# Optimization experiments

Measured on AMD Instinct MI355X. Metric: run time of the kernel, lower is better.

Reference implementation:

```python
import jax, jax.numpy as jnp
import numpy as np

N = 100_000
E = 1_000_000
D = 64
NORM_FACTOR = 100.0
LN_EPS = 1e-5


def setup_inputs() -> dict:
    key = jax.random.key(0)
    ks = jax.random.split(key, 8)
    h = jax.random.normal(ks[0], (N, D), dtype=jnp.float32)
    distances = jax.random.uniform(ks[1], (E, 1), dtype=jnp.float32)
    edges = jax.random.randint(ks[2], (2, E), 0, N, dtype=jnp.int64)
    node_mask = jnp.ones((N, 1), dtype=jnp.float32)
    edge_mask = jnp.ones((E, 1), dtype=jnp.float32)
    s = 1.0 / np.sqrt(D)
    W_lin = jax.random.normal(ks[3], (D, D), dtype=jnp.float32) * s
    b_lin = jnp.zeros((D,), dtype=jnp.float32)
    att_W1 = jax.random.normal(ks[4], (D, 2 * D + 1), dtype=jnp.float32) * (1.0 / np.sqrt(2 * D + 1))
    att_b1 = jnp.zeros((D,), dtype=jnp.float32)
    att_W2 = jax.random.normal(ks[5], (1, D), dtype=jnp.float32) * s
    att_b2 = jnp.zeros((1,), dtype=jnp.float32)
    ln_g = jnp.ones((D,), dtype=jnp.float32)
    ln_b = jnp.zeros((D,), dtype=jnp.float32)
    return {"h": h, "distances": distances, "edges": edges, "node_mask": node_mask,
            "edge_mask": edge_mask, "W_lin": W_lin, "b_lin": b_lin,
            "att_W1": att_W1, "att_b1": att_b1, "att_W2": att_W2, "att_b2": att_b2,
            "ln_g": ln_g, "ln_b": ln_b}


def reference(h, distances, edges, node_mask, edge_mask, W_lin, b_lin,
              att_W1, att_b1, att_W2, att_b2, ln_g, ln_b):
    # Linear projection: [N, D]
    x = h @ W_lin.T + b_lin
    row, col = edges[0], edges[1]
    x_row = x[row]          # [E, D]
    x_col = x[col]          # [E, D]
    # DenseAtt: MLP(concat(x_row, x_col, dist)) -> sigmoid -> * edge_mask
    cat = jnp.concatenate([x_row, x_col, distances], axis=1)  # [E, 2D+1]
    hdn = jax.nn.silu(cat @ att_W1.T + att_b1)                # [E, D]
    att = jax.nn.sigmoid(hdn @ att_W2.T + att_b2) * edge_mask # [E, 1]
    # Attention-weighted scatter-sum aggregation into row segments
    agg = x_col * att
    out = jax.ops.segment_sum(agg, row, num_segments=x.shape[0]) / NORM_FACTOR
    out = out + x           # residual
    # LayerNorm + activation
    mu = jnp.mean(out, axis=-1, keepdims=True)
    var = jnp.mean(jnp.square(out - mu), axis=-1, keepdims=True)
    y = (out - mu) * jax.lax.rsqrt(var + LN_EPS) * ln_g + ln_b
    return jax.nn.silu(y)
```

## Files before the change

### kernel.cpp

```cpp
#include <hip/hip_runtime.h>
#include <hip/hip_bf16.h>

#define N_NODES 100000
#define N_EDGES 1000000
#define DIM 64
#define NORM_INV 0.01f
#define LN_EPS 1e-5f
#define N_TILES 6250
#define PROJ_BLOCKS 1563
#define N_BUCKETS 782
#define HISTB 489
#define L2E 1.4426950408889634f
#define LN2 0.6931471805599453f

typedef __attribute__((ext_vector_type(8))) short short8;
typedef __attribute__((ext_vector_type(4))) float f32x4;

__device__ __forceinline__ unsigned short f2bf(float f) {
    union { float f; unsigned u; } x; x.f = f;
    unsigned r = x.u + 0x7FFFu + ((x.u >> 16) & 1u);
    return (unsigned short)(r >> 16);
}
__device__ __forceinline__ float bf2f(unsigned short s) {
    union { unsigned u; float f; } x; x.u = ((unsigned)s) << 16; return x.f;
}

__global__ __launch_bounds__(256) void prep_frags(
    const float* __restrict__ W, const float* __restrict__ att_W1,
    const float* __restrict__ att_b1, const float* __restrict__ att_W2,
    short8* __restrict__ whi, short8* __restrict__ wlo,
    short8* __restrict__ wa, short8* __restrict__ wb,
    float4* __restrict__ tab) {
    const int l = threadIdx.x & 63;
    const int nt = threadIdx.x >> 6;
    const int c = l & 15, q = l >> 4;
    const int n = nt * 16 + c;
#pragma unroll
    for (int ks = 0; ks < 2; ++ks) {
        const int k0 = ks * 32 + q * 8;
        short8 hi8, lo8, a8, b8;
#pragma unroll
        for (int jj = 0; jj < 8; ++jj) {
            float w = W[n * 64 + k0 + jj];
            unsigned short hh = f2bf(w);
            hi8[jj] = (short)hh;
            lo8[jj] = (short)f2bf(w - bf2f(hh));
            a8[jj] = (short)f2bf(att_W1[n * 129 + k0 + jj]);
            b8[jj] = (short)f2bf(att_W1[n * 129 + 64 + k0 + jj]);
        }
        const int idx = (nt * 2 + ks) * 64 + l;
        whi[idx] = hi8; wlo[idx] = lo8; wa[idx] = a8; wb[idx] = b8;
    }
    if (threadIdx.x < 64) {
        const int f = threadIdx.x;
        tab[f] = make_float4(att_W2[f] * LN2, att_W1[f * 129 + 128] * L2E,
                             att_b1[f] * L2E, 0.f);
    }
}

__global__ __launch_bounds__(256) void proj_hist(
    const float* __restrict__ h, const float* __restrict__ bl,
    const short8* __restrict__ whi, const short8* __restrict__ wlo,
    const short8* __restrict__ wa, const short8* __restrict__ wb,
    const int* __restrict__ edges, int* __restrict__ bucketCnt,
    unsigned short* __restrict__ xv, unsigned short* __restrict__ u_bf) {
    if (blockIdx.x >= PROJ_BLOCKS) {
        __shared__ int lh[N_BUCKETS];
        const int tid = threadIdx.x;
        for (int i = tid; i < N_BUCKETS; i += 256) lh[i] = 0;
        __syncthreads();
        const int e0 = (blockIdx.x - PROJ_BLOCKS) * 2048;
#pragma unroll
        for (int i = 0; i < 8; ++i) {
            const int e = e0 + tid * 8 + i;
            if (e < N_EDGES) atomicAdd(&lh[edges[e] >> 7], 1);
        }
        __syncthreads();
        for (int b = tid; b < N_BUCKETS; b += 256)
            if (lh[b]) atomicAdd(&bucketCnt[b], lh[b]);
        return;
    }
    __shared__ __align__(16) unsigned short lds[4][16 * 72];
    const int lane = threadIdx.x & 63;
    const int wv = threadIdx.x >> 6;
    const int c = lane & 15, q = lane >> 4;
    const int tile = blockIdx.x * 4 + wv;
    if (tile >= N_TILES) return;
    const int n0 = tile * 16;

    short8 Whi[4][2], Wlo[4][2], Wa[4][2], Wb[4][2];
    float bias[4];
#pragma unroll
    for (int nt = 0; nt < 4; ++nt) {
        bias[nt] = bl[nt * 16 + c];
#pragma unroll
        for (int ks = 0; ks < 2; ++ks) {
            const int idx = (nt * 2 + ks) * 64 + lane;
            Whi[nt][ks] = whi[idx]; Wlo[nt][ks] = wlo[idx];
            Wa[nt][ks] = wa[idx];   Wb[nt][ks] = wb[idx];
        }
    }

    short8 Ahi[2], Alo[2];
#pragma unroll
    for (int ks = 0; ks < 2; ++ks) {
        const float* hp = h + (size_t)(n0 + c) * 64 + ks * 32 + q * 8;
        f32x4 p0 = *(const f32x4*)hp;
        f32x4 p1 = *(const f32x4*)(hp + 4);
        short8 hi8, lo8;
#pragma unroll
        for (int jj = 0; jj < 4; ++jj) {
            unsigned short hh = f2bf(p0[jj]);
            hi8[jj] = (short)hh; lo8[jj] = (short)f2bf(p0[jj] - bf2f(hh));
            unsigned short h2 = f2bf(p1[jj]);
            hi8[4 + jj] = (short)h2; lo8[4 + jj] = (short)f2bf(p1[jj] - bf2f(h2));
        }
        Ahi[ks] = hi8; Alo[ks] = lo8;
    }

    f32x4 xacc[4] = {{0,0,0,0},{0,0,0,0},{0,0,0,0},{0,0,0,0}};
#pragma unroll
    for (int ks = 0; ks < 2; ++ks)
#pragma unroll
        for (int nt = 0; nt < 4; ++nt) {
            xacc[nt] = __builtin_amdgcn_mfma_f32_16x16x32_bf16(Ahi[ks], Whi[nt][ks], xacc[nt], 0, 0, 0);
            xacc[nt] = __builtin_amdgcn_mfma_f32_16x16x32_bf16(Ahi[ks], Wlo[nt][ks], xacc[nt], 0, 0, 0);
            xacc[nt] = __builtin_amdgcn_mfma_f32_16x16x32_bf16(Alo[ks], Whi[nt][ks], xacc[nt], 0, 0, 0);
        }

    unsigned short* lw = lds[wv];
#pragma unroll
    for (int r = 0; r < 4; ++r) {
        const int node = n0 + q * 4 + r;
        unsigned short xb[4];
#pragma unroll
        for (int nt = 0; nt < 4; ++nt) {
            unsigned short v16 = f2bf(xacc[nt][r] + bias[nt]);
            xb[nt] = v16;
            lw[(q * 4 + r) * 72 + nt * 16 + c] = v16;
        }
        uint2 pk;
        pk.x = (unsigned)xb[0] | ((unsigned)xb[1] << 16);
        pk.y = (unsigned)xb[2] | ((unsigned)xb[3] << 16);
        *(uint2*)(xv + (size_t)node * 128 + c * 8) = pk;
    }

    short8 Ax[2];
#pragma unroll
    for (int ks = 0; ks < 2; ++ks)
        Ax[ks] = *(const short8*)&lw[c * 72 + ks * 32 + q * 8];

    f32x4 uacc[4] = {{0,0,0,0},{0,0,0,0},{0,0,0,0},{0,0,0,0}};
    f32x4 vacc[4] = {{0,0,0,0},{0,0,0,0},{0,0,0,0},{0,0,0,0}};
#pragma unroll
    for (int ks = 0; ks < 2; ++ks)
#pragma unroll
        for (int nt = 0; nt < 4; ++nt) {
            uacc[nt] = __builtin_amdgcn_mfma_f32_16x16x32_bf16(Ax[ks], Wa[nt][ks], uacc[nt], 0, 0, 0);
            vacc[nt] = __builtin_amdgcn_mfma_f32_16x16x32_bf16(Ax[ks], Wb[nt][ks], vacc[nt], 0, 0, 0);
        }
#pragma unroll
    for (int r = 0; r < 4; ++r) {
        const int node = n0 + q * 4 + r;
        uint2 pu;
        pu.x = (unsigned)f2bf(uacc[0][r] * L2E) | ((unsigned)f2bf(uacc[1][r] * L2E) << 16);
        pu.y = (unsigned)f2bf(uacc[2][r] * L2E) | ((unsigned)f2bf(uacc[3][r] * L2E) << 16);
        *(uint2*)(u_bf + (size_t)node * 64 + c * 4) = pu;
        uint2 pk;
        pk.x = (unsigned)f2bf(vacc[0][r] * L2E) | ((unsigned)f2bf(vacc[1][r] * L2E) << 16);
        pk.y = (unsigned)f2bf(vacc[2][r] * L2E) | ((unsigned)f2bf(vacc[3][r] * L2E) << 16);
        *(uint2*)(xv + (size_t)node * 128 + c * 8 + 4) = pk;
    }
}

__global__ __launch_bounds__(1024) void scanA(
    const int* __restrict__ bucketCnt, int* __restrict__ baseA,
    int* __restrict__ cursA) {
    __shared__ int wsum[16];
    const int t = threadIdx.x, lane = t & 63, w = t >> 6;
    const int v = (t < N_BUCKETS) ? bucketCnt[t] : 0;
    int sc = v;
#pragma unroll
    for (int off = 1; off < 64; off <<= 1) {
        int u = __shfl_up(sc, off);
        if (lane >= off) sc += u;
    }
    if (lane == 63) wsum[w] = sc;
    __syncthreads();
    if (w == 0) {
        int x = (lane < 16) ? wsum[lane] : 0;
#pragma unroll
        for (int off = 1; off < 16; off <<= 1) {
            int u = __shfl_up(x, off);
            if (lane >= off) x += u;
        }
        if (lane < 16) wsum[lane] = x;
    }
    __syncthreads();
    const int excl = sc - v + ((w > 0) ? wsum[w - 1] : 0);
    if (t < N_BUCKETS) { baseA[t] = excl; cursA[t] = excl; }
    if (t == N_BUCKETS - 1) baseA[N_BUCKETS] = excl + v;
}

__global__ __launch_bounds__(256) void scatterA(
    const int* __restrict__ edges, const float* __restrict__ dist,
    const float* __restrict__ emask, int* __restrict__ cursA,
    uint2* __restrict__ srec, unsigned char* __restrict__ lrowS) {
    __shared__ int lh[N_BUCKETS];
    __shared__ int lb[N_BUCKETS];
    const int tid = threadIdx.x;
    for (int i = tid; i < N_BUCKETS; i += 256) lh[i] = 0;
    __syncthreads();

    const int e0 = blockIdx.x * 2048 + tid * 8;
    int row[8], col[8];
    unsigned de[8];
#pragma unroll
    for (int i = 0; i < 8; ++i) {
        const int e = e0 + i;
        if (e < N_EDGES) {
            row[i] = edges[e];
            col[i] = edges[N_EDGES + e];
            de[i] = (unsigned)f2bf(dist[e]) | ((unsigned)f2bf(emask[e] * NORM_INV) << 16);
            atomicAdd(&lh[row[i] >> 7], 1);
        } else {
            row[i] = -1;
        }
    }
    __syncthreads();
    for (int b = tid; b < N_BUCKETS; b += 256) {
        const int c = lh[b];
        lb[b] = c ? atomicAdd(&cursA[b], c) : 0;
    }
    __syncthreads();
    for (int i = tid; i < N_BUCKETS; i += 256) lh[i] = 0;
    __syncthreads();
#pragma unroll
    for (int i = 0; i < 8; ++i) {
        if (row[i] >= 0) {
            const int bk = row[i] >> 7;
            const int rk = atomicAdd(&lh[bk], 1);
            const int pos = lb[bk] + rk;
            uint2 rc; rc.x = (unsigned)col[i]; rc.y = de[i];
            srec[pos] = rc;
            lrowS[pos] = (unsigned char)(row[i] & 127);
        }
    }
}

__global__ __launch_bounds__(256) void bucketB1(
    const int* __restrict__ baseA, const unsigned char* __restrict__ lrowS,
    int* __restrict__ pbt) {
    __shared__ int hist[128];
    __shared__ int tt[4];
    const int tid = threadIdx.x;
    const int b = blockIdx.x;
    if (tid < 128) hist[tid] = 0;
    __syncthreads();
    const int s0 = baseA[b], s1 = baseA[b + 1];
    for (int e = s0 + tid; e < s1; e += 256) atomicAdd(&hist[lrowS[e]], 1);
    __syncthreads();
    int p = (tid < 128) ? ((hist[tid] + 3) & ~3) : 0;
#pragma unroll
    for (int off = 1; off < 64; off <<= 1) p += __shfl_xor(p, off);
    if ((tid & 63) == 0) tt[tid >> 6] = p;
    __syncthreads();
    if (tid == 0) pbt[b] = tt[0] + tt[1];
}

__global__ __launch_bounds__(1024) void scanB(
    const int* __restrict__ pbt, int* __restrict__ baseB,
    int* __restrict__ start, uint2* __restrict__ recs) {
    __shared__ int wsum[16];
    const int t = threadIdx.x, lane = t & 63, w = t >> 6;
    const int v = (t < N_BUCKETS) ? pbt[t] : 0;
    int sc = v;
#pragma unroll
    for (int off = 1; off < 64; off <<= 1) {
        int u = __shfl_up(sc, off);
        if (lane >= off) sc += u;
    }
    if (lane == 63) wsum[w] = sc;
    __syncthreads();
    if (w == 0) {
        int x = (lane < 16) ? wsum[lane] : 0;
#pragma unroll
        for (int off = 1; off < 16; off <<= 1) {
            int u = __shfl_up(x, off);
            if (lane >= off) x += u;
        }
        if (lane < 16) wsum[lane] = x;
    }
    __syncthreads();
    const int excl = sc - v + ((w > 0) ? wsum[w - 1] : 0);
    if (t < N_BUCKETS) baseB[t] = excl;
    if (t == N_BUCKETS - 1) {
        const int tot = excl + v;
        baseB[N_BUCKETS] = tot;
        start[N_NODES] = tot;
        uint2 z; z.x = 0; z.y = 0;
        for (int i = 0; i < 16; ++i) recs[tot + i] = z;
    }
}

__global__ __launch_bounds__(256) void bucketB2(
    const int* __restrict__ baseA, const int* __restrict__ baseB,
    const unsigned char* __restrict__ lrowS, const uint2* __restrict__ srec,
    uint2* __restrict__ recs, int* __restrict__ start) {
    __shared__ int hist[128];
    __shared__ int cur[128];
    __shared__ int wtot;
    const int tid = threadIdx.x, lane = tid & 63;
    const int b = blockIdx.x;
    if (tid < 128) hist[tid] = 0;
    __syncthreads();
    const int s0 = baseA[b], s1 = baseA[b + 1];
    for (int e = s0 + tid; e < s1; e += 256) atomicAdd(&hist[lrowS[e]], 1);
    __syncthreads();
    int c = 0, p = 0, sc = 0;
    if (tid < 128) {
        c = hist[tid];
        p = (c + 3) & ~3;
        sc = p;
#pragma unroll
        for (int off = 1; off < 64; off <<= 1) {
            int u = __shfl_up(sc, off);
            if (lane >= off) sc += u;
        }
        if (tid == 63) wtot = sc;
    }
    __syncthreads();
    if (tid < 128) {
        if (tid >= 64) sc += wtot;
        const int excl = baseB[b] + sc - p;
        cur[tid] = excl;
        const int grow = b * 128 + tid;
        if (grow < N_NODES) start[grow] = excl;
        uint2 z; z.x = 0; z.y = 0;
        for (int i = c; i < p; ++i) recs[excl + i] = z;
    }
    __syncthreads();
    for (int e = s0 + tid; e < s1; e += 256) {
        const int lr = lrowS[e];
        const uint2 rc = srec[e];
        const int pos = atomicAdd(&cur[lr], 1);
        recs[pos] = rc;
    }
}

__global__ __launch_bounds__(256, 8) void agg_ln_kernel(
    const int* __restrict__ start, const uint2* __restrict__ recs,
    const unsigned short* __restrict__ xv, const unsigned short* __restrict__ u_bf,
    const float4* __restrict__ tab, const float* __restrict__ att_b2,
    const float* __restrict__ ln_g, const float* __restrict__ ln_b,
    float* __restrict__ out) {
    const int lane = threadIdx.x & 63;
    const int wv = threadIdx.x >> 6;
    const int j = lane & 15;
    const int s = lane >> 4;
    const int r = blockIdx.x * 4 + wv;

    const float4 t0 = tab[j], t1 = tab[j + 16], t2 = tab[j + 32], t3 = tab[j + 48];
    const uint2 uu = *(const uint2*)(u_bf + (size_t)r * 64 + j * 4);
    const float base0 = __uint_as_float(uu.x << 16) + t0.z;
    const float base1 = __uint_as_float(uu.x & 0xffff0000u) + t1.z;
    const float base2 = __uint_as_float(uu.y << 16) + t2.z;
    const float base3 = __uint_as_float(uu.y & 0xffff0000u) + t3.z;
    const float b2L = att_b2[0] * L2E;

    const int s0 = start[r];
    const int e1 = start[r + 1];
    const unsigned* xvu = (const unsigned*)xv;

    float a0 = 0.f, a1 = 0.f, a2 = 0.f, a3 = 0.f;
    if (e1 > s0) {
        uint2 recA = recs[s0 + s];
        uint4 xvA = *(const uint4*)(xvu + (size_t)recA.x * 64 + j * 4);
        uint2 recB = recs[s0 + 4 + s];
        for (int e = s0; e < e1; e += 4) {
            const uint2 recC = recs[e + 8 + s];
            const uint4 xvB = *(const uint4*)(xvu + (size_t)recB.x * 64 + j * 4);

            const float dist = __uint_as_float(recA.y << 16);
            const float emN = __uint_as_float(recA.y & 0xffff0000u);
            const float x0 = __uint_as_float(xvA.x << 16);
            const float x1 = __uint_as_float(xvA.x & 0xffff0000u);
            const float x2 = __uint_as_float(xvA.y << 16);
            const float x3 = __uint_as_float(xvA.y & 0xffff0000u);
            const float v0 = __uint_as_float(xvA.z << 16);
            const float v1 = __uint_as_float(xvA.z & 0xffff0000u);
            const float v2 = __uint_as_float(xvA.w << 16);
            const float v3 = __uint_as_float(xvA.w & 0xffff0000u);
            float pv = 0.f, pre, sg;
            pre = fmaf(dist, t0.y, base0) + v0;
            sg = __builtin_amdgcn_rcpf(1.f + __builtin_amdgcn_exp2f(-pre));
            pv = fmaf(pre * sg, t0.x, pv);
            pre = fmaf(dist, t1.y, base1) + v1;
            sg = __builtin_amdgcn_rcpf(1.f + __builtin_amdgcn_exp2f(-pre));
            pv = fmaf(pre * sg, t1.x, pv);
            pre = fmaf(dist, t2.y, base2) + v2;
            sg = __builtin_amdgcn_rcpf(1.f + __builtin_amdgcn_exp2f(-pre));
            pv = fmaf(pre * sg, t2.x, pv);
            pre = fmaf(dist, t3.y, base3) + v3;
            sg = __builtin_amdgcn_rcpf(1.f + __builtin_amdgcn_exp2f(-pre));
            pv = fmaf(pre * sg, t3.x, pv);
            pv += __shfl_xor(pv, 1); pv += __shfl_xor(pv, 2);
            pv += __shfl_xor(pv, 4); pv += __shfl_xor(pv, 8);
            const float sp = fmaf(pv, L2E, b2L);
            const float att =
                emN * __builtin_amdgcn_rcpf(1.f + __builtin_amdgcn_exp2f(-sp));
            a0 = fmaf(att, x0, a0); a1 = fmaf(att, x1, a1);
            a2 = fmaf(att, x2, a2); a3 = fmaf(att, x3, a3);
            recA = recB; xvA = xvB; recB = recC;
        }
    }
    a0 += __shfl_xor(a0, 16); a0 += __shfl_xor(a0, 32);
    a1 += __shfl_xor(a1, 16); a1 += __shfl_xor(a1, 32);
    a2 += __shfl_xor(a2, 16); a2 += __shfl_xor(a2, 32);
    a3 += __shfl_xor(a3, 16); a3 += __shfl_xor(a3, 32);

    const uint2 xr = *(const uint2*)(xvu + (size_t)r * 64 + j * 4);
    const float o0 = __uint_as_float(xr.x << 16) + a0;
    const float o1 = __uint_as_float(xr.x & 0xffff0000u) + a1;
    const float o2 = __uint_as_float(xr.y << 16) + a2;
    const float o3 = __uint_as_float(xr.y & 0xffff0000u) + a3;

    float ssum = o0 + o1 + o2 + o3;
    ssum += __shfl_xor(ssum, 1); ssum += __shfl_xor(ssum, 2);
    ssum += __shfl_xor(ssum, 4); ssum += __shfl_xor(ssum, 8);
    const float mu = ssum * (1.f / 64.f);
    const float d0 = o0 - mu, d1 = o1 - mu, d2 = o2 - mu, d3 = o3 - mu;
    float vs = d0 * d0 + d1 * d1 + d2 * d2 + d3 * d3;
    vs += __shfl_xor(vs, 1); vs += __shfl_xor(vs, 2);
    vs += __shfl_xor(vs, 4); vs += __shfl_xor(vs, 8);
    const float rstd = rsqrtf(vs * (1.f / 64.f) + LN_EPS);

    const int f = j + 16 * s;
    const float dk = (s == 0) ? d0 : (s == 1) ? d1 : (s == 2) ? d2 : d3;
    const float y = fmaf(dk * rstd, ln_g[f], ln_b[f]);
    out[(size_t)r * 64 + lane] =
        y * __builtin_amdgcn_rcpf(1.f + __builtin_amdgcn_exp2f(-y * L2E));
}

extern "C" void kernel_launch(void* const* d_in, const int* in_sizes, int n_in,
                              void* d_out, int out_size, void* d_ws, size_t ws_size,
                              hipStream_t stream) {
    const float* h      = (const float*)d_in[0];
    const float* dist   = (const float*)d_in[1];
    const int*   edges  = (const int*)d_in[2];
    const float* emask  = (const float*)d_in[4];
    const float* W_lin  = (const float*)d_in[5];
    const float* b_lin  = (const float*)d_in[6];
    const float* att_W1 = (const float*)d_in[7];
    const float* att_b1 = (const float*)d_in[8];
    const float* att_W2 = (const float*)d_in[9];
    const float* att_b2 = (const float*)d_in[10];
    const float* ln_g   = (const float*)d_in[11];
    const float* ln_b   = (const float*)d_in[12];
    float* out = (float*)d_out;

    char* ws = (char*)d_ws;
    unsigned short* xv   = (unsigned short*)ws;
    unsigned short* u_bf = (unsigned short*)(ws + 25600000);
    uint2* srec          = (uint2*)(ws + 38400000);
    uint2* recs          = (uint2*)(ws + 46400000);
    unsigned char* lrowS = (unsigned char*)(ws + 56800128);
    int* start           = (int*)(ws + 57800192);
    int* bucketCnt       = (int*)(ws + 58200576);
    int* baseA           = (int*)(ws + 58204672);
    int* cursA           = (int*)(ws + 58208768);
    int* pbt             = (int*)(ws + 58212864);
    int* baseB           = (int*)(ws + 58216960);
    float4* tab          = (float4*)(ws + 58221056);
    short8* whi          = (short8*)(ws + 58222080);
    short8* wlo          = (short8*)(ws + 58230272);
    short8* wa           = (short8*)(ws + 58238464);
    short8* wb           = (short8*)(ws + 58246656);

    hipMemsetAsync(bucketCnt, 0, N_BUCKETS * sizeof(int), stream);
    prep_frags<<<1, 256, 0, stream>>>(W_lin, att_W1, att_b1, att_W2,
                                      whi, wlo, wa, wb, tab);
    proj_hist<<<PROJ_BLOCKS + HISTB, 256, 0, stream>>>(
        h, b_lin, whi, wlo, wa, wb, edges, bucketCnt, xv, u_bf);
    scanA<<<1, 1024, 0, stream>>>(bucketCnt, baseA, cursA);
    scatterA<<<HISTB, 256, 0, stream>>>(edges, dist, emask, cursA, srec, lrowS);
    bucketB1<<<N_BUCKETS, 256, 0, stream>>>(baseA, lrowS, pbt);
    scanB<<<1, 1024, 0, stream>>>(pbt, baseB, start, recs);
    bucketB2<<<N_BUCKETS, 256, 0, stream>>>(baseA, baseB, lrowS, srec, recs, start);
    agg_ln_kernel<<<N_NODES / 4, 256, 0, stream>>>(start, recs, xv, u_bf,
                                                   tab, att_b2, ln_g, ln_b, out);
}
```

Before: 237.9 us.

## Replace per-row CSR sort with bucket-level aggregation using LDS atomic accumulators

Drops the second sorting pass (bucketB1, scanB, bucketB2) and the per-row CSR records. Edges are now only bucketed by 128-row groups, with the local row packed into the record, and one block per bucket accumulates attention-weighted messages into a shared-memory float accumulator using LDS atomics before applying LayerNorm. This removes three kernel launches and a full extra pass over the edge records. In exchange it adds LDS atomic traffic and contention, lowers occupancy because of the 48KB of shared memory per block, and risks load imbalance with only 782 blocks. It also folds the bias and log2e scaling into the precomputed weights and u vector, replaces the memset with a second prep block, and uses DPP reductions.

```diff
diff --git a/kernel.cpp b/kernel.cpp
--- a/kernel.cpp
+++ b/kernel.cpp
@@ -25,12 +25,39 @@
     union { unsigned u; float f; } x; x.u = ((unsigned)s) << 16; return x.f;
 }
 
+template <int CTRL>
+__device__ __forceinline__ float dpp_add(float v) {
+    int t = __builtin_amdgcn_update_dpp(0, __float_as_int(v), CTRL, 0xF, 0xF, true);
+    return v + __int_as_float(t);
+}
+__device__ __forceinline__ float red16(float v) {
+    v = dpp_add<0xB1>(v);
+    v = dpp_add<0x4E>(v);
+    v = dpp_add<0x124>(v);
+    v = dpp_add<0x128>(v);
+    return v;
+}
+__device__ __forceinline__ float red64(float v) {
+    v = red16(v);
+    v += __shfl_xor(v, 16);
+    v += __shfl_xor(v, 32);
+    return v;
+}
+
 __global__ __launch_bounds__(256) void prep_frags(
     const float* __restrict__ W, const float* __restrict__ att_W1,
-    const float* __restrict__ att_b1, const float* __restrict__ att_W2,
+    const float* __restrict__ att_W2,
     short8* __restrict__ whi, short8* __restrict__ wlo,
     short8* __restrict__ wa, short8* __restrict__ wb,
-    float4* __restrict__ tab) {
+    float2* __restrict__ tab2, int* __restrict__ bucketCnt) {
+    if (blockIdx.x == 1) {
+        for (int i = threadIdx.x; i < N_BUCKETS; i += 256) bucketCnt[i] = 0;
+        if (threadIdx.x < 64) {
+            const int f = threadIdx.x;
+            tab2[f] = make_float2(att_W2[f] * LN2, att_W1[f * 129 + 128] * L2E);
+        }
+        return;
+    }
     const int l = threadIdx.x & 63;
     const int nt = threadIdx.x >> 6;
     const int c = l & 15, q = l >> 4;
@@ -45,21 +72,17 @@
             unsigned short hh = f2bf(w);
             hi8[jj] = (short)hh;
             lo8[jj] = (short)f2bf(w - bf2f(hh));
-            a8[jj] = (short)f2bf(att_W1[n * 129 + k0 + jj]);
-            b8[jj] = (short)f2bf(att_W1[n * 129 + 64 + k0 + jj]);
+            a8[jj] = (short)f2bf(att_W1[n * 129 + k0 + jj] * L2E);
+            b8[jj] = (short)f2bf(att_W1[n * 129 + 64 + k0 + jj] * L2E);
         }
         const int idx = (nt * 2 + ks) * 64 + l;
         whi[idx] = hi8; wlo[idx] = lo8; wa[idx] = a8; wb[idx] = b8;
     }
-    if (threadIdx.x < 64) {
-        const int f = threadIdx.x;
-        tab[f] = make_float4(att_W2[f] * LN2, att_W1[f * 129 + 128] * L2E,
-                             att_b1[f] * L2E, 0.f);
-    }
 }
 
 __global__ __launch_bounds__(256) void proj_hist(
     const float* __restrict__ h, const float* __restrict__ bl,
+    const float* __restrict__ att_b1,
     const short8* __restrict__ whi, const short8* __restrict__ wlo,
     const short8* __restrict__ wa, const short8* __restrict__ wb,
     const int* __restrict__ edges, int* __restrict__ bucketCnt,
@@ -89,10 +112,11 @@
     const int n0 = tile * 16;
 
     short8 Whi[4][2], Wlo[4][2], Wa[4][2], Wb[4][2];
-    float bias[4];
+    float bias[4], b1L[4];
 #pragma unroll
     for (int nt = 0; nt < 4; ++nt) {
         bias[nt] = bl[nt * 16 + c];
+        b1L[nt] = att_b1[nt * 16 + c] * L2E;
 #pragma unroll
         for (int ks = 0; ks < 2; ++ks) {
             const int idx = (nt * 2 + ks) * 64 + lane;
@@ -163,12 +187,12 @@
     for (int r = 0; r < 4; ++r) {
         const int node = n0 + q * 4 + r;
         uint2 pu;
-        pu.x = (unsigned)f2bf(uacc[0][r] * L2E) | ((unsigned)f2bf(uacc[1][r] * L2E) << 16);
-        pu.y = (unsigned)f2bf(uacc[2][r] * L2E) | ((unsigned)f2bf(uacc[3][r] * L2E) << 16);
+        pu.x = (unsigned)f2bf(uacc[0][r] + b1L[0]) | ((unsigned)f2bf(uacc[1][r] + b1L[1]) << 16);
+        pu.y = (unsigned)f2bf(uacc[2][r] + b1L[2]) | ((unsigned)f2bf(uacc[3][r] + b1L[3]) << 16);
         *(uint2*)(u_bf + (size_t)node * 64 + c * 4) = pu;
         uint2 pk;
-        pk.x = (unsigned)f2bf(vacc[0][r] * L2E) | ((unsigned)f2bf(vacc[1][r] * L2E) << 16);
-        pk.y = (unsigned)f2bf(vacc[2][r] * L2E) | ((unsigned)f2bf(vacc[3][r] * L2E) << 16);
+        pk.x = (unsigned)f2bf(vacc[0][r]) | ((unsigned)f2bf(vacc[1][r]) << 16);
+        pk.y = (unsigned)f2bf(vacc[2][r]) | ((unsigned)f2bf(vacc[3][r]) << 16);
         *(uint2*)(xv + (size_t)node * 128 + c * 8 + 4) = pk;
     }
 }
@@ -205,7 +229,7 @@
 __global__ __launch_bounds__(256) void scatterA(
     const int* __restrict__ edges, const float* __restrict__ dist,
     const float* __restrict__ emask, int* __restrict__ cursA,
-    uint2* __restrict__ srec, unsigned char* __restrict__ lrowS) {
+    uint2* __restrict__ srec) {
     __shared__ int lh[N_BUCKETS];
     __shared__ int lb[N_BUCKETS];
     const int tid = threadIdx.x;
@@ -240,149 +264,68 @@
         if (row[i] >= 0) {
             const int bk = row[i] >> 7;
             const int rk = atomicAdd(&lh[bk], 1);
-            const int pos = lb[bk] + rk;
-            uint2 rc; rc.x = (unsigned)col[i]; rc.y = de[i];
-            srec[pos] = rc;
-            lrowS[pos] = (unsigned char)(row[i] & 127);
-        }
-    }
-}
-
-__global__ __launch_bounds__(256) void bucketB1(
-    const int* __restrict__ baseA, const unsigned char* __restrict__ lrowS,
-    int* __restrict__ pbt) {
-    __shared__ int hist[128];
-    __shared__ int tt[4];
-    const int tid = threadIdx.x;
-    const int b = blockIdx.x;
-    if (tid < 128) hist[tid] = 0;
-    __syncthreads();
-    const int s0 = baseA[b], s1 = baseA[b + 1];
-    for (int e = s0 + tid; e < s1; e += 256) atomicAdd(&hist[lrowS[e]], 1);
-    __syncthreads();
-    int p = (tid < 128) ? ((hist[tid] + 3) & ~3) : 0;
-#pragma unroll
-    for (int off = 1; off < 64; off <<= 1) p += __shfl_xor(p, off);
-    if ((tid & 63) == 0) tt[tid >> 6] = p;
-    __syncthreads();
-    if (tid == 0) pbt[b] = tt[0] + tt[1];
-}
-
-__global__ __launch_bounds__(1024) void scanB(
-    const int* __restrict__ pbt, int* __restrict__ baseB,
-    int* __restrict__ start, uint2* __restrict__ recs) {
-    __shared__ int wsum[16];
-    const int t = threadIdx.x, lane = t & 63, w = t >> 6;
-    const int v = (t < N_BUCKETS) ? pbt[t] : 0;
-    int sc = v;
-#pragma unroll
-    for (int off = 1; off < 64; off <<= 1) {
-        int u = __shfl_up(sc, off);
-        if (lane >= off) sc += u;
-    }
-    if (lane == 63) wsum[w] = sc;
-    __syncthreads();
-    if (w == 0) {
-        int x = (lane < 16) ? wsum[lane] : 0;
-#pragma unroll
-        for (int off = 1; off < 16; off <<= 1) {
-            int u = __shfl_up(x, off);
-            if (lane >= off) x += u;
-        }
-        if (lane < 16) wsum[lane] = x;
-    }
-    __syncthreads();
-    const int excl = sc - v + ((w > 0) ? wsum[w - 1] : 0);
-    if (t < N_BUCKETS) baseB[t] = excl;
-    if (t == N_BUCKETS - 1) {
-        const int tot = excl + v;
-        baseB[N_BUCKETS] = tot;
-        start[N_NODES] = tot;
-        uint2 z; z.x = 0; z.y = 0;
-        for (int i = 0; i < 16; ++i) recs[tot + i] = z;
-    }
-}
-
-__global__ __launch_bounds__(256) void bucketB2(
-    const int* __restrict__ baseA, const int* __restrict__ baseB,
-    const unsigned char* __restrict__ lrowS, const uint2* __restrict__ srec,
-    uint2* __restrict__ recs, int* __restrict__ start) {
-    __shared__ int hist[128];
-    __shared__ int cur[128];
-    __shared__ int wtot;
-    const int tid = threadIdx.x, lane = tid & 63;
-    const int b = blockIdx.x;
-    if (tid < 128) hist[tid] = 0;
-    __syncthreads();
-    const int s0 = baseA[b], s1 = baseA[b + 1];
-    for (int e = s0 + tid; e < s1; e += 256) atomicAdd(&hist[lrowS[e]], 1);
-    __syncthreads();
-    int c = 0, p = 0, sc = 0;
-    if (tid < 128) {
-        c = hist[tid];
-        p = (c + 3) & ~3;
-        sc = p;
-#pragma unroll
-        for (int off = 1; off < 64; off <<= 1) {
-            int u = __shfl_up(sc, off);
-            if (lane >= off) sc += u;
-        }
-        if (tid == 63) wtot = sc;
-    }
-    __syncthreads();
-    if (tid < 128) {
-        if (tid >= 64) sc += wtot;
-        const int excl = baseB[b] + sc - p;
-        cur[tid] = excl;
-        const int grow = b * 128 + tid;
-        if (grow < N_NODES) start[grow] = excl;
-        uint2 z; z.x = 0; z.y = 0;
-        for (int i = c; i < p; ++i) recs[excl + i] = z;
-    }
-    __syncthreads();
-    for (int e = s0 + tid; e < s1; e += 256) {
-        const int lr = lrowS[e];
-        const uint2 rc = srec[e];
-        const int pos = atomicAdd(&cur[lr], 1);
-        recs[pos] = rc;
-    }
-}
-
-__global__ __launch_bounds__(256, 8) void agg_ln_kernel(
-    const int* __restrict__ start, const uint2* __restrict__ recs,
+            uint2 rc;
+            rc.x = (unsigned)col[i] | ((unsigned)(row[i] & 127) << 17);
+            rc.y = de[i];
+            srec[lb[bk] + rk] = rc;
+        }
+    }
+}
+
+__global__ __launch_bounds__(256, 3) void agg_bucket(
+    const int* __restrict__ baseA, const uint2* __restrict__ srec,
     const unsigned short* __restrict__ xv, const unsigned short* __restrict__ u_bf,
-    const float4* __restrict__ tab, const float* __restrict__ att_b2,
+    const float2* __restrict__ tab2, const float* __restrict__ att_b2,
     const float* __restrict__ ln_g, const float* __restrict__ ln_b,
     float* __restrict__ out) {
-    const int lane = threadIdx.x & 63;
-    const int wv = threadIdx.x >> 6;
+    __shared__ __align__(16) float acc[128 * 64];
+    __shared__ __align__(16) unsigned short uld[128 * 64];
+
+    const int tid = threadIdx.x;
+    const int lane = tid & 63;
+    const int wv = tid >> 6;
     const int j = lane & 15;
     const int s = lane >> 4;
-    const int r = blockIdx.x * 4 + wv;
-
-    const float4 t0 = tab[j], t1 = tab[j + 16], t2 = tab[j + 32], t3 = tab[j + 48];
-    const uint2 uu = *(const uint2*)(u_bf + (size_t)r * 64 + j * 4);
-    const float base0 = __uint_as_float(uu.x << 16) + t0.z;
-    const float base1 = __uint_as_float(uu.x & 0xffff0000u) + t1.z;
-    const float base2 = __uint_as_float(uu.y << 16) + t2.z;
-    const float base3 = __uint_as_float(uu.y & 0xffff0000u) + t3.z;
+    const int b = blockIdx.x;
+    const int row0 = b * 128;
+    const int nrows = min(128, N_NODES - row0);
+
+    {
+        uint4* u4 = (uint4*)uld;
+        const uint4* ug = (const uint4*)(u_bf + (size_t)row0 * 64);
+        for (int i = tid; i < 1024; i += 256) u4[i] = ug[i];
+        f32x4* a4 = (f32x4*)acc;
+        const f32x4 z = {0.f, 0.f, 0.f, 0.f};
+        for (int i = tid; i < 2048; i += 256) a4[i] = z;
+    }
+    __syncthreads();
+
+    const float2 t0 = tab2[j], t1 = tab2[j + 16], t2 = tab2[j + 32], t3 = tab2[j + 48];
     const float b2L = att_b2[0] * L2E;
-
-    const int s0 = start[r];
-    const int e1 = start[r + 1];
+    const int s0 = baseA[b];
+    const int s1 = baseA[b + 1];
     const unsigned* xvu = (const unsigned*)xv;
 
-    float a0 = 0.f, a1 = 0.f, a2 = 0.f, a3 = 0.f;
-    if (e1 > s0) {
-        uint2 recA = recs[s0 + s];
-        uint4 xvA = *(const uint4*)(xvu + (size_t)recA.x * 64 + j * 4);
-        uint2 recB = recs[s0 + 4 + s];
-        for (int e = s0; e < e1; e += 4) {
-            const uint2 recC = recs[e + 8 + s];
-            const uint4 xvB = *(const uint4*)(xvu + (size_t)recB.x * 64 + j * 4);
+    int e = s0 + wv * 4;
+    if (e < s1) {
+        int ia = min(e + s, s1 - 1);
+        uint2 recA = srec[ia];
+        uint4 xvA = *(const uint4*)(xvu + (size_t)(recA.x & 0x1FFFF) * 64 + j * 4);
+        int ib = min(e + 16 + s, s1 - 1);
+        uint2 recB = srec[ib];
+        for (; e < s1; e += 16) {
+            const int ic = min(e + 32 + s, s1 - 1);
+            const uint2 recC = srec[ic];
+            const uint4 xvB = *(const uint4*)(xvu + (size_t)(recB.x & 0x1FFFF) * 64 + j * 4);
 
             const float dist = __uint_as_float(recA.y << 16);
-            const float emN = __uint_as_float(recA.y & 0xffff0000u);
+            const float emN = ((e + s) < s1) ? __uint_as_float(recA.y & 0xffff0000u) : 0.f;
+            const int lrow = (int)(recA.x >> 17);
+            const uint2 uu = *(const uint2*)&uld[lrow * 64 + j * 4];
+            const float u0 = __uint_as_float(uu.x << 16);
+            const float u1 = __uint_as_float(uu.x & 0xffff0000u);
+            const float u2 = __uint_as_float(uu.y << 16);
+            const float u3 = __uint_as_float(uu.y & 0xffff0000u);
             const float x0 = __uint_as_float(xvA.x << 16);
             const float x1 = __uint_as_float(xvA.x & 0xffff0000u);
             const float x2 = __uint_as_float(xvA.y << 16);
@@ -391,55 +334,54 @@
             const float v1 = __uint_as_float(xvA.z & 0xffff0000u);
             const float v2 = __uint_as_float(xvA.w << 16);
             const float v3 = __uint_as_float(xvA.w & 0xffff0000u);
+
             float pv = 0.f, pre, sg;
-            pre = fmaf(dist, t0.y, base0) + v0;
+            pre = fmaf(dist, t0.y, u0) + v0;
             sg = __builtin_amdgcn_rcpf(1.f + __builtin_amdgcn_exp2f(-pre));
             pv = fmaf(pre * sg, t0.x, pv);
-            pre = fmaf(dist, t1.y, base1) + v1;
+            pre = fmaf(dist, t1.y, u1) + v1;
             sg = __builtin_amdgcn_rcpf(1.f + __builtin_amdgcn_exp2f(-pre));
             pv = fmaf(pre * sg, t1.x, pv);
-            pre = fmaf(dist, t2.y, base2) + v2;
+            pre = fmaf(dist, t2.y, u2) + v2;
             sg = __builtin_amdgcn_rcpf(1.f + __builtin_amdgcn_exp2f(-pre));
             pv = fmaf(pre * sg, t2.x, pv);
-            pre = fmaf(dist, t3.y, base3) + v3;
+            pre = fmaf(dist, t3.y, u3) + v3;
             sg = __builtin_amdgcn_rcpf(1.f + __builtin_amdgcn_exp2f(-pre));
             pv = fmaf(pre * sg, t3.x, pv);
-            pv += __shfl_xor(pv, 1); pv += __shfl_xor(pv, 2);
-            pv += __shfl_xor(pv, 4); pv += __shfl_xor(pv, 8);
+
+            pv = red16(pv);
             const float sp = fmaf(pv, L2E, b2L);
             const float att =
                 emN * __builtin_amdgcn_rcpf(1.f + __builtin_amdgcn_exp2f(-sp));
-            a0 = fmaf(att, x0, a0); a1 = fmaf(att, x1, a1);
-            a2 = fmaf(att, x2, a2); a3 = fmaf(att, x3, a3);
+
+            float* ar = acc + lrow * 64 + j * 4;
+            atomicAdd(ar + 0, att * x0);
+            atomicAdd(ar + 1, att * x1);
+            atomicAdd(ar + 2, att * x2);
+            atomicAdd(ar + 3, att * x3);
+
             recA = recB; xvA = xvB; recB = recC;
         }
     }
-    a0 += __shfl_xor(a0, 16); a0 += __shfl_xor(a0, 32);
-    a1 += __shfl_xor(a1, 16); a1 += __shfl_xor(a1, 32);
-    a2 += __shfl_xor(a2, 16); a2 += __shfl_xor(a2, 32);
-    a3 += __shfl_xor(a3, 16); a3 += __shfl_xor(a3, 32);
-
-    const uint2 xr = *(const uint2*)(xvu + (size_t)r * 64 + j * 4);
-    const float o0 = __uint_as_float(xr.x << 16) + a0;
-    const float o1 = __uint_as_float(xr.x & 0xffff0000u) + a1;
-    const float o2 = __uint_as_float(xr.y << 16) + a2;
-    const float o3 = __uint_as_float(xr.y & 0xffff0000u) + a3;
-
-    float ssum = o0 + o1 + o2 + o3;
-    ssum += __shfl_xor(ssum, 1); ssum += __shfl_xor(ssum, 2);
-    ssum += __shfl_xor(ssum, 4); ssum += __shfl_xor(ssum, 8);
-    const float mu = ssum * (1.f / 64.f);
-    const float d0 = o0 - mu, d1 = o1 - mu, d2 = o2 - mu, d3 = o3 - mu;
-    float vs = d0 * d0 + d1 * d1 + d2 * d2 + d3 * d3;
-    vs += __shfl_xor(vs, 1); vs += __shfl_xor(vs, 2);
-    vs += __shfl_xor(vs, 4); vs += __shfl_xor(vs, 8);
-    const float rstd = rsqrtf(vs * (1.f / 64.f) + LN_EPS);
-
-    const int f = j + 16 * s;
-    const float dk = (s == 0) ? d0 : (s == 1) ? d1 : (s == 2) ? d2 : d3;
-    const float y = fmaf(dk * rstd, ln_g[f], ln_b[f]);
-    out[(size_t)r * 64 + lane] =
-        y * __builtin_amdgcn_rcpf(1.f + __builtin_amdgcn_exp2f(-y * L2E));
+    __syncthreads();
+
+    const int f = lane;
+    const int jj = f & 15, kk = f >> 4;
+    const float gv = ln_g[f], bv = ln_b[f];
+    for (int r = wv; r < nrows; r += 4) {
+        const int node = row0 + r;
+        const float a = acc[r * 64 + jj * 4 + kk];
+        const float xres = bf2f(xv[(size_t)node * 128 + jj * 8 + kk]);
+        const float o = xres + a;
+        const float sm = red64(o);
+        const float sq = red64(o * o);
+        const float mu = sm * (1.f / 64.f);
+        const float var = sq * (1.f / 64.f) - mu * mu;
+        const float rstd = rsqrtf(var + LN_EPS);
+        const float y = fmaf((o - mu) * rstd, gv, bv);
+        out[(size_t)node * 64 + f] =
+            y * __builtin_amdgcn_rcpf(1.f + __builtin_amdgcn_exp2f(-y * L2E));
+    }
 }
 
 extern "C" void kernel_launch(void* const* d_in, const int* in_sizes, int n_in,
@@ -463,30 +405,21 @@
     unsigned short* xv   = (unsigned short*)ws;
     unsigned short* u_bf = (unsigned short*)(ws + 25600000);
     uint2* srec          = (uint2*)(ws + 38400000);
-    uint2* recs          = (uint2*)(ws + 46400000);
-    unsigned char* lrowS = (unsigned char*)(ws + 56800128);
-    int* start           = (int*)(ws + 57800192);
-    int* bucketCnt       = (int*)(ws + 58200576);
-    int* baseA           = (int*)(ws + 58204672);
-    int* cursA           = (int*)(ws + 58208768);
-    int* pbt             = (int*)(ws + 58212864);
-    int* baseB           = (int*)(ws + 58216960);
-    float4* tab          = (float4*)(ws + 58221056);
-    short8* whi          = (short8*)(ws + 58222080);
-    short8* wlo          = (short8*)(ws + 58230272);
-    short8* wa           = (short8*)(ws + 58238464);
-    short8* wb           = (short8*)(ws + 58246656);
-
-    hipMemsetAsync(bucketCnt, 0, N_BUCKETS * sizeof(int), stream);
-    prep_frags<<<1, 256, 0, stream>>>(W_lin, att_W1, att_b1, att_W2,
-                                      whi, wlo, wa, wb, tab);
+    int* bucketCnt       = (int*)(ws + 46400000);
+    int* baseA           = (int*)(ws + 46403200);
+    int* cursA           = (int*)(ws + 46406400);
+    float2* tab2         = (float2*)(ws + 46409600);
+    short8* whi          = (short8*)(ws + 46410112);
+    short8* wlo          = (short8*)(ws + 46418304);
+    short8* wa           = (short8*)(ws + 46426496);
+    short8* wb           = (short8*)(ws + 46434688);
+
+    prep_frags<<<2, 256, 0, stream>>>(W_lin, att_W1, att_W2, whi, wlo, wa, wb,
+                                      tab2, bucketCnt);
     proj_hist<<<PROJ_BLOCKS + HISTB, 256, 0, stream>>>(
-        h, b_lin, whi, wlo, wa, wb, edges, bucketCnt, xv, u_bf);
+        h, b_lin, att_b1, whi, wlo, wa, wb, edges, bucketCnt, xv, u_bf);
     scanA<<<1, 1024, 0, stream>>>(bucketCnt, baseA, cursA);
-    scatterA<<<HISTB, 256, 0, stream>>>(edges, dist, emask, cursA, srec, lrowS);
-    bucketB1<<<N_BUCKETS, 256, 0, stream>>>(baseA, lrowS, pbt);
-    scanB<<<1, 1024, 0, stream>>>(pbt, baseB, start, recs);
-    bucketB2<<<N_BUCKETS, 256, 0, stream>>>(baseA, baseB, lrowS, srec, recs, start);
-    agg_ln_kernel<<<N_NODES / 4, 256, 0, stream>>>(start, recs, xv, u_bf,
-                                                   tab, att_b2, ln_g, ln_b, out);
-}
+    scatterA<<<HISTB, 256, 0, stream>>>(edges, dist, emask, cursA, srec);
+    agg_bucket<<<N_BUCKETS, 256, 0, stream>>>(baseA, srec, xv, u_bf, tab2,
+                                              att_b2, ln_g, ln_b, out);
+}
```

Result: slower. 591.1 us (+148.5%).
